# Optimization experiments

Hardware: AMD Instinct MI355X
Metric: run time of the kernel (lower is better)

## Reference

```python
import jax, jax.numpy as jnp
import numpy as np


def setup_inputs() -> dict:
    key = jax.random.key(0)
    B, n = 1048576, 8
    x = jax.random.normal(key, (B, n, n), dtype=jnp.float32)
    return {"x": x, "num_iters": 5}


def reference(x, num_iters):
    # FusedMHC.forward: flatten to [B, n, n] in fp32, run Sinkhorn, cast back.
    input_dtype = x.dtype
    n = x.shape[-1]
    M = jnp.exp(x.reshape(-1, n, n).astype(jnp.float32))  # positive kernel matrix
    # num_iters alternating row / column normalizations (Sinkhorn-Knopp)
    for _ in range(num_iters):
        M = M / jnp.sum(M, axis=-1, keepdims=True)  # row normalize
        M = M / jnp.sum(M, axis=-2, keepdims=True)  # col normalize
    return M.reshape(x.shape).astype(input_dtype)
```

## Files before the change

kernel.cpp:

```cpp
#include <hip/hip_runtime.h>


#define N 8

__global__ __launch_bounds__(256) void sinkhorn8_kernel(
    const float* __restrict__ x,
    float* __restrict__ out,
    const int* __restrict__ num_iters_p,
    int B)
{
    int b = blockIdx.x * blockDim.x + threadIdx.x;
    if (b >= B) return;

    const int num_iters = *num_iters_p;

    const float4* __restrict__ xv = (const float4*)(x + (size_t)b * (N * N));
    float4* __restrict__ ov = (float4*)(out + (size_t)b * (N * N));

    float M[N * N];

#pragma unroll
    for (int k = 0; k < 16; ++k) {
        float4 v = xv[k];
        M[4 * k + 0] = __expf(v.x);
        M[4 * k + 1] = __expf(v.y);
        M[4 * k + 2] = __expf(v.z);
        M[4 * k + 3] = __expf(v.w);
    }

    for (int it = 0; it < num_iters; ++it) {
#pragma unroll
        for (int r = 0; r < N; ++r) {
            float s = 0.f;
#pragma unroll
            for (int c = 0; c < N; ++c) s += M[r * N + c];
            float inv = __builtin_amdgcn_rcpf(s);
#pragma unroll
            for (int c = 0; c < N; ++c) M[r * N + c] *= inv;
        }
#pragma unroll
        for (int c = 0; c < N; ++c) {
            float s = 0.f;
#pragma unroll
            for (int r = 0; r < N; ++r) s += M[r * N + c];
            float inv = __builtin_amdgcn_rcpf(s);
#pragma unroll
            for (int r = 0; r < N; ++r) M[r * N + c] *= inv;
        }
    }

#pragma unroll
    for (int k = 0; k < 16; ++k) {
        float4 v;
        v.x = M[4 * k + 0];
        v.y = M[4 * k + 1];
        v.z = M[4 * k + 2];
        v.w = M[4 * k + 3];
        ov[k] = v;
    }
}

extern "C" void kernel_launch(void* const* d_in, const int* in_sizes, int n_in,
                              void* d_out, int out_size, void* d_ws, size_t ws_size,
                              hipStream_t stream) {
    const float* x = (const float*)d_in[0];
    const int* num_iters = (const int*)d_in[1];
    float* out = (float*)d_out;

    int B = in_sizes[0] / (N * N);
    int block = 256;
    int grid = (B + block - 1) / block;

    sinkhorn8_kernel<<<grid, block, 0, stream>>>(x, out, num_iters, B);
}
```

Before: 451.4 us.

## Stage matrices through swizzled LDS for coalesced global loads and stores

Each block now loads its 256 matrices with fully coalesced float4 reads into a 64KB shared buffer using an XOR swizzle, then each thread reads its own matrix from LDS. The output goes back the same way: written to LDS, then stored coalesced to global memory. This replaces the strided per-thread 256-byte accesses that spread each wavefront over many cache lines. In exchange it adds LDS traffic and two barriers, and 64KB of LDS per block limits occupancy, which may weaken latency hiding.

```diff
diff --git a/kernel.cpp b/kernel.cpp
--- a/kernel.cpp
+++ b/kernel.cpp
@@ -2,26 +2,40 @@
 
 
 #define N 8
+#define TPB 256
 
-__global__ __launch_bounds__(256) void sinkhorn8_kernel(
+__global__ __launch_bounds__(TPB) void sinkhorn8_kernel(
     const float* __restrict__ x,
     float* __restrict__ out,
     const int* __restrict__ num_iters_p,
-    int B)
+    int nF4)
 {
-    int b = blockIdx.x * blockDim.x + threadIdx.x;
-    if (b >= B) return;
+    __shared__ float4 lds[TPB * 16];
 
+    const int t = threadIdx.x;
+    const size_t blockBase = (size_t)blockIdx.x * (TPB * 16);
     const int num_iters = *num_iters_p;
 
-    const float4* __restrict__ xv = (const float4*)(x + (size_t)b * (N * N));
-    float4* __restrict__ ov = (float4*)(out + (size_t)b * (N * N));
-
-    float M[N * N];
+    const float4* __restrict__ xv = (const float4*)x;
+    float4* __restrict__ ov = (float4*)out;
 
 #pragma unroll
     for (int k = 0; k < 16; ++k) {
-        float4 v = xv[k];
+        size_t f = blockBase + t + k * TPB;
+        if (f < (size_t)nF4) {
+            float4 v = xv[f];
+            int fl = t + k * TPB;
+            int m  = fl >> 4;
+            int k4 = fl & 15;
+            lds[(m << 4) | (k4 ^ (m & 15))] = v;
+        }
+    }
+    __syncthreads();
+
+    float M[N * N];
+#pragma unroll
+    for (int k = 0; k < 16; ++k) {
+        float4 v = lds[(t << 4) | (k ^ (t & 15))];
         M[4 * k + 0] = __expf(v.x);
         M[4 * k + 1] = __expf(v.y);
         M[4 * k + 2] = __expf(v.z);
@@ -56,7 +70,19 @@
         v.y = M[4 * k + 1];
         v.z = M[4 * k + 2];
         v.w = M[4 * k + 3];
-        ov[k] = v;
+        lds[(t << 4) | (k ^ (t & 15))] = v;
+    }
+    __syncthreads();
+
+#pragma unroll
+    for (int k = 0; k < 16; ++k) {
+        size_t f = blockBase + t + k * TPB;
+        if (f < (size_t)nF4) {
+            int fl = t + k * TPB;
+            int m  = fl >> 4;
+            int k4 = fl & 15;
+            ov[f] = lds[(m << 4) | (k4 ^ (m & 15))];
+        }
     }
 }
 
@@ -67,9 +93,9 @@
     const int* num_iters = (const int*)d_in[1];
     float* out = (float*)d_out;
 
+    int nF4 = in_sizes[0] / 4;
     int B = in_sizes[0] / (N * N);
-    int block = 256;
-    int grid = (B + block - 1) / block;
+    int grid = (B + TPB - 1) / TPB;
 
-    sinkhorn8_kernel<<<grid, block, 0, stream>>>(x, out, num_iters, B);
+    sinkhorn8_kernel<<<grid, TPB, 0, stream>>>(x, out, num_iters, nF4);
 }
```

New measurement: 456.4 us. Within noise of the previous version (+1.1%).
